# Optimization experiments

Measured on AMD Instinct MI355X. Metric: run time of the kernel, lower is better.

## Reference

```python
import jax, jax.numpy as jnp
import numpy as np

N_NODES = 100000
N_EDGES = 1600000
N_GRAPHS = 256
NODE_F = 92
EDGE_F = 41
HID = 64


def setup_inputs() -> dict:
    key = jax.random.key(0)
    ks = jax.random.split(key, 16)
    Z = 2 * HID + EDGE_F  # 169, concat dim for CGConv
    inp = {
        "x": jax.random.normal(ks[0], (N_NODES, NODE_F), dtype=jnp.float32),
        "edge_index": jax.random.randint(ks[1], (2, N_EDGES), 0, N_NODES, dtype=jnp.int64),
        "edge_attr": jax.random.uniform(ks[2], (N_EDGES, EDGE_F), dtype=jnp.float32),
        "batch": jnp.sort(jax.random.randint(ks[3], (N_NODES,), 0, N_GRAPHS, dtype=jnp.int64)),
        # embedding Linear(node_feat_dim -> hidden)
        "emb_W": jax.random.normal(ks[4], (NODE_F, HID), dtype=jnp.float32) / np.sqrt(NODE_F),
        "emb_b": jnp.zeros((HID,), dtype=jnp.float32),
        # CGConv layer 1: gate (sigmoid) and source (softplus) linears on z=[x_i,x_j,e]
        "c1_Wf": jax.random.normal(ks[5], (Z, HID), dtype=jnp.float32) / np.sqrt(Z),
        "c1_bf": jnp.zeros((HID,), dtype=jnp.float32),
        "c1_Ws": jax.random.normal(ks[6], (Z, HID), dtype=jnp.float32) / np.sqrt(Z),
        "c1_bs": jnp.zeros((HID,), dtype=jnp.float32),
        # CGConv layer 2
        "c2_Wf": jax.random.normal(ks[7], (Z, HID), dtype=jnp.float32) / np.sqrt(Z),
        "c2_bf": jnp.zeros((HID,), dtype=jnp.float32),
        "c2_Ws": jax.random.normal(ks[8], (Z, HID), dtype=jnp.float32) / np.sqrt(Z),
        "c2_bs": jnp.zeros((HID,), dtype=jnp.float32),
        # head
        "l1_W": jax.random.normal(ks[9], (HID, 32), dtype=jnp.float32) / np.sqrt(HID),
        "l1_b": jnp.zeros((32,), dtype=jnp.float32),
        "l2_W": jax.random.normal(ks[10], (32, 2), dtype=jnp.float32) / np.sqrt(32),
        "l2_b": jnp.zeros((2,), dtype=jnp.float32),
    }
    return inp


def _cgconv(x, src, dst, edge_attr, Wf, bf, Ws, bs):
    # PyG CGConv: z = [x_i (target), x_j (source), e_ij]; msg = sigmoid(lin_f(z)) * softplus(lin_s(z))
    z = jnp.concatenate([x[dst], x[src], edge_attr], axis=-1)  # [E, 2H+D]
    msg = jax.nn.sigmoid(z @ Wf + bf) * jax.nn.softplus(z @ Ws + bs)  # [E, H]
    agg = jax.ops.segment_sum(msg, dst, num_segments=x.shape[0])  # scatter-add at targets
    return x + agg  # residual


def reference(x, edge_index, edge_attr, batch,
              emb_W, emb_b, c1_Wf, c1_bf, c1_Ws, c1_bs,
              c2_Wf, c2_bf, c2_Ws, c2_bs, l1_W, l1_b, l2_W, l2_b):
    src = edge_index[0]  # x_j
    dst = edge_index[1]  # x_i
    h = jax.nn.relu(x @ emb_W + emb_b)
    h = jax.nn.relu(_cgconv(h, src, dst, edge_attr, c1_Wf, c1_bf, c1_Ws, c1_bs))
    h = jax.nn.relu(_cgconv(h, src, dst, edge_attr, c2_Wf, c2_bf, c2_Ws, c2_bs))
    # global_mean_pool over graph ids
    sums = jax.ops.segment_sum(h, batch, num_segments=N_GRAPHS)
    cnt = jax.ops.segment_sum(jnp.ones((h.shape[0],), h.dtype), batch, num_segments=N_GRAPHS)
    pooled = sums / jnp.maximum(cnt, 1.0)[:, None]
    g = jax.nn.relu(pooled @ l1_W + l1_b)
    return g @ l2_W + l2_b  # [N_GRAPHS, 2]
```

## Files before the change

kernel.cpp:

```cpp
#include <hip/hip_runtime.h>

#define N_NODES 100000
#define N_EDGES 1600000
#define N_GRAPHS 256
#define NODE_F 92
#define EDGE_F 41
#define HID 64
#define NCHUNK 98

typedef float f2 __attribute__((ext_vector_type(2)));
typedef float f4 __attribute__((ext_vector_type(4)));

__global__ __launch_bounds__(256) void k_embed(const float* __restrict__ x,
                                               const float* __restrict__ W,
                                               const float* __restrict__ b,
                                               float* __restrict__ h) {
    __shared__ float sT[23 * 256];
    for (int i = threadIdx.x; i < 23 * 256; i += 256) {
        const int kq = i >> 8, rem = i & 255, ln = rem >> 2, kk = rem & 3;
        sT[i] = W[(4 * kq + kk) * HID + ln];
    }
    __syncthreads();
    const int lane = threadIdx.x & 63;
    const int nW   = gridDim.x * 4;
    const float bias = b[lane];
    for (int n0 = blockIdx.x * 4 + (threadIdx.x >> 6); n0 < N_NODES; n0 += nW) {
        const int n = __builtin_amdgcn_readfirstlane(n0);
        const float* xr = x + (size_t)n * NODE_F;
        float acc = bias;
#pragma unroll
        for (int k0 = 0; k0 < NODE_F; k0 += 4) {
            const f4 xv = *(const f4*)&xr[k0];
            const f4 wv = *(const f4*)&sT[(k0 >> 2) * 256 + 4 * lane];
            acc = fmaf(xv.x, wv.x, acc);
            acc = fmaf(xv.y, wv.y, acc);
            acc = fmaf(xv.z, wv.z, acc);
            acc = fmaf(xv.w, wv.w, acc);
        }
        h[(size_t)n * HID + lane] = fmaxf(acc, 0.f);
    }
}

__global__ __launch_bounds__(256) void k_hist(const int* __restrict__ ei,
                                              int* __restrict__ cnt) {
    for (int i = blockIdx.x * 256 + threadIdx.x; i < N_EDGES; i += gridDim.x * 256)
        atomicAdd(&cnt[ei[N_EDGES + i]], 1);
}

__global__ __launch_bounds__(256) void k_scan1(const int* __restrict__ cnt,
                                               int* __restrict__ csum) {
    __shared__ int red[256];
    const int b = blockIdx.x, t = threadIdx.x;
    int s = 0;
    for (int i = t; i < 1024; i += 256) {
        const int g = b * 1024 + i;
        s += (g < N_NODES) ? cnt[g] : 0;
    }
    red[t] = s;
    __syncthreads();
    for (int off = 128; off > 0; off >>= 1) {
        if (t < off) red[t] += red[t + off];
        __syncthreads();
    }
    if (t == 0) csum[b] = red[0];
}

__global__ __launch_bounds__(128) void k_scan2(const int* __restrict__ csum,
                                               int* __restrict__ cbase) {
    __shared__ int sh[128];
    const int t = threadIdx.x;
    const int v0 = (t < NCHUNK) ? csum[t] : 0;
    sh[t] = v0;
    __syncthreads();
    for (int off = 1; off < 128; off <<= 1) {
        const int v = (t >= off) ? sh[t - off] : 0;
        __syncthreads();
        sh[t] += v;
        __syncthreads();
    }
    if (t < NCHUNK) cbase[t] = sh[t] - v0;
}

__global__ __launch_bounds__(256) void k_scan3(const int* __restrict__ cnt,
                                               const int* __restrict__ cbase,
                                               int* __restrict__ offs,
                                               int* __restrict__ woffs) {
    __shared__ int sh[256];
    const int b = blockIdx.x, t = threadIdx.x;
    const int g0 = b * 1024 + t * 4;
    int v[4], s = 0;
#pragma unroll
    for (int k = 0; k < 4; ++k) {
        const int g = g0 + k;
        v[k] = (g < N_NODES) ? cnt[g] : 0;
        s += v[k];
    }
    sh[t] = s;
    __syncthreads();
    for (int off = 1; off < 256; off <<= 1) {
        const int x = (t >= off) ? sh[t - off] : 0;
        __syncthreads();
        sh[t] += x;
        __syncthreads();
    }
    int base = cbase[b] + sh[t] - s;
#pragma unroll
    for (int k = 0; k < 4; ++k) {
        const int g = g0 + k;
        if (g < N_NODES) { offs[g] = base; woffs[g] = base; }
        base += v[k];
    }
    if (b == 0 && t == 0) offs[N_NODES] = N_EDGES;
}

__global__ __launch_bounds__(256) void k_scatter(const int* __restrict__ ei,
                                                 int* __restrict__ woffs,
                                                 int2* __restrict__ csr) {
    for (int i = blockIdx.x * 256 + threadIdx.x; i < N_EDGES; i += gridDim.x * 256) {
        const int src = ei[i];
        const int dst = ei[N_EDGES + i];
        const int pos = atomicAdd(&woffs[dst], 1);
        csr[pos] = make_int2(src, i);
    }
}

template <int RELU_IN>
__global__ __launch_bounds__(256) void k_node_pre(const float* hin,
                                                  float* hout,
                                                  const float* __restrict__ Wf,
                                                  const float* __restrict__ Ws,
                                                  float* __restrict__ D,
                                                  float* __restrict__ S) {
    __shared__ float sW[64 * 256];
    for (int i = threadIdx.x; i < 64 * 256; i += 256) {
        const int k = i >> 8, j = i & 255, c = j >> 2, r = j & 3;
        float v;
        if (r == 0)      v = Wf[k * HID + c];
        else if (r == 1) v = Ws[k * HID + c];
        else if (r == 2) v = Wf[(64 + k) * HID + c];
        else             v = Ws[(64 + k) * HID + c];
        sW[i] = v;
    }
    __syncthreads();
    const int lane = threadIdx.x & 63;
    const int wave = blockIdx.x * 4 + (threadIdx.x >> 6);
    const int nW   = gridDim.x * 4;
    for (int base0 = wave * 8; base0 < N_NODES; base0 += nW * 8) {
        const int base = __builtin_amdgcn_readfirstlane(base0);
        float aD0[8] = {}, aD1[8] = {}, aS0[8] = {}, aS1[8] = {};
        for (int k0 = 0; k0 < HID; k0 += 4) {
            f4 wv[4];
#pragma unroll
            for (int kk = 0; kk < 4; ++kk)
                wv[kk] = *(const f4*)&sW[(k0 + kk) * 256 + 4 * lane];
#pragma unroll
            for (int m = 0; m < 8; ++m) {
                f4 hv = *(const f4*)&hin[(size_t)(base + m) * HID + k0];
                if (RELU_IN) {
                    hv.x = fmaxf(hv.x, 0.f); hv.y = fmaxf(hv.y, 0.f);
                    hv.z = fmaxf(hv.z, 0.f); hv.w = fmaxf(hv.w, 0.f);
                }
#pragma unroll
                for (int kk = 0; kk < 4; ++kk) {
                    aD0[m] = fmaf(hv[kk], wv[kk].x, aD0[m]);
                    aD1[m] = fmaf(hv[kk], wv[kk].y, aD1[m]);
                    aS0[m] = fmaf(hv[kk], wv[kk].z, aS0[m]);
                    aS1[m] = fmaf(hv[kk], wv[kk].w, aS1[m]);
                }
            }
        }
#pragma unroll
        for (int m = 0; m < 8; ++m) {
            const size_t n = base + m;
            *(f2*)&D[n * 128 + 2 * lane] = (f2){aD0[m], aD1[m]};
            *(f2*)&S[n * 128 + 2 * lane] = (f2){aS0[m], aS1[m]};
            if (RELU_IN) hout[n * HID + lane] = fmaxf(hin[n * HID + lane], 0.f);
        }
    }
}

__device__ __forceinline__ float act(float f, float s) {
    const float gate = __builtin_amdgcn_rcpf(1.f + __expf(-f));
    const float sp   = fmaxf(s, 0.f) + __logf(1.f + __expf(-fabsf(s)));
    return gate * sp;
}

__global__ __launch_bounds__(256, 4) void k_gather(const int2* __restrict__ csr,
                                                   const int* __restrict__ offs,
                                                   const float* __restrict__ ea,
                                                   const float* __restrict__ D,
                                                   const float* __restrict__ S,
                                                   const float* __restrict__ Wf,
                                                   const float* __restrict__ Ws,
                                                   const float* __restrict__ bf,
                                                   const float* __restrict__ bs,
                                                   const float* hres,
                                                   float* agg) {
    const int lane = threadIdx.x & 63;
    float wf[EDGE_F], ws[EDGE_F];
#pragma unroll
    for (int k = 0; k < EDGE_F; ++k) {
        wf[k] = Wf[(128 + k) * HID + lane];
        ws[k] = Ws[(128 + k) * HID + lane];
    }
    const float bfv = bf[lane], bsv = bs[lane];
    const int nW = gridDim.x * 4;
    for (int n0 = blockIdx.x * 4 + (threadIdx.x >> 6); n0 < N_NODES; n0 += nW) {
        const int n  = __builtin_amdgcn_readfirstlane(n0);
        const int j0 = offs[n];
        const int j1 = offs[n + 1];
        float acc = hres[(size_t)n * HID + lane];
        const f2 dv = *(const f2*)&D[(size_t)n * 128 + 2 * lane];
        const float bD0 = bfv + dv.x, bD1 = bsv + dv.y;
        int j = j0;
        for (; j + 1 < j1; j += 2) {
            const int2 c0 = csr[j], c1 = csr[j + 1];
            const int s0 = __builtin_amdgcn_readfirstlane(c0.x);
            const int e0 = __builtin_amdgcn_readfirstlane(c0.y);
            const int s1 = __builtin_amdgcn_readfirstlane(c1.x);
            const int e1 = __builtin_amdgcn_readfirstlane(c1.y);
            const f2 sv0 = *(const f2*)&S[(size_t)s0 * 128 + 2 * lane];
            const f2 sv1 = *(const f2*)&S[(size_t)s1 * 128 + 2 * lane];
            const float* r0 = ea + (size_t)e0 * EDGE_F;
            const float* r1 = ea + (size_t)e1 * EDGE_F;
            float f0 = bD0 + sv0.x, q0 = bD1 + sv0.y;
            float f1 = bD0 + sv1.x, q1 = bD1 + sv1.y;
#pragma unroll
            for (int k = 0; k < EDGE_F; ++k) {
                const float a = r0[k], b = r1[k];
                f0 = fmaf(a, wf[k], f0); q0 = fmaf(a, ws[k], q0);
                f1 = fmaf(b, wf[k], f1); q1 = fmaf(b, ws[k], q1);
            }
            acc += act(f0, q0) + act(f1, q1);
        }
        if (j < j1) {
            const int2 c0 = csr[j];
            const int s0 = __builtin_amdgcn_readfirstlane(c0.x);
            const int e0 = __builtin_amdgcn_readfirstlane(c0.y);
            const f2 sv0 = *(const f2*)&S[(size_t)s0 * 128 + 2 * lane];
            const float* r0 = ea + (size_t)e0 * EDGE_F;
            float f0 = bD0 + sv0.x, q0 = bD1 + sv0.y;
#pragma unroll
            for (int k = 0; k < EDGE_F; ++k) {
                const float a = r0[k];
                f0 = fmaf(a, wf[k], f0); q0 = fmaf(a, ws[k], q0);
            }
            acc += act(f0, q0);
        }
        agg[(size_t)n * HID + lane] = acc;
    }
}

__global__ __launch_bounds__(256) void k_pool(const float* __restrict__ agg,
                                              const int* __restrict__ batch,
                                              float* __restrict__ psum,
                                              float* __restrict__ pcnt) {
    const int lane = threadIdx.x & 63;
    const int wave = blockIdx.x * 4 + (threadIdx.x >> 6);
    const int nW   = gridDim.x * 4;
    const int chunk = (N_NODES + nW - 1) / nW;
    const int n0 = wave * chunk;
    if (n0 >= N_NODES) return;
    const int n1 = min(n0 + chunk, N_NODES);
    float acc = 0.f;
    int cur = batch[n0];
    int run = 0;
    for (int n = n0; n < n1; ++n) {
        const int g = batch[n];
        if (g != cur) {
            unsafeAtomicAdd(&psum[(size_t)cur * HID + lane], acc);
            if (lane == 0) unsafeAtomicAdd(&pcnt[cur], (float)run);
            acc = 0.f; run = 0; cur = g;
        }
        acc += fmaxf(agg[(size_t)n * HID + lane], 0.f);
        ++run;
    }
    unsafeAtomicAdd(&psum[(size_t)cur * HID + lane], acc);
    if (lane == 0) unsafeAtomicAdd(&pcnt[cur], (float)run);
}

__global__ __launch_bounds__(256) void k_head(const float* __restrict__ psum,
                                              const float* __restrict__ pcnt,
                                              const float* __restrict__ l1W,
                                              const float* __restrict__ l1b,
                                              const float* __restrict__ l2W,
                                              const float* __restrict__ l2b,
                                              float* __restrict__ out) {
    const int g = threadIdx.x;
    const float inv = 1.f / fmaxf(pcnt[g], 1.f);
    float hid[32];
#pragma unroll
    for (int j = 0; j < 32; ++j) hid[j] = l1b[j];
    for (int c = 0; c < HID; ++c) {
        const float pv = psum[(size_t)g * HID + c] * inv;
#pragma unroll
        for (int j = 0; j < 32; ++j) hid[j] = fmaf(pv, l1W[c * 32 + j], hid[j]);
    }
#pragma unroll
    for (int j = 0; j < 32; ++j) hid[j] = fmaxf(hid[j], 0.f);
#pragma unroll
    for (int k = 0; k < 2; ++k) {
        float a = l2b[k];
#pragma unroll
        for (int j = 0; j < 32; ++j) a = fmaf(hid[j], l2W[j * 2 + k], a);
        out[g * 2 + k] = a;
    }
}

extern "C" void kernel_launch(void* const* d_in, const int* in_sizes, int n_in,
                              void* d_out, int out_size, void* d_ws, size_t ws_size,
                              hipStream_t stream) {
    const float* x     = (const float*)d_in[0];
    const int*   ei    = (const int*)d_in[1];
    const float* ea    = (const float*)d_in[2];
    const int*   batch = (const int*)d_in[3];
    const float* embW  = (const float*)d_in[4];
    const float* embb  = (const float*)d_in[5];
    const float* c1Wf  = (const float*)d_in[6];
    const float* c1bf  = (const float*)d_in[7];
    const float* c1Ws  = (const float*)d_in[8];
    const float* c1bs  = (const float*)d_in[9];
    const float* c2Wf  = (const float*)d_in[10];
    const float* c2bf  = (const float*)d_in[11];
    const float* c2Ws  = (const float*)d_in[12];
    const float* c2bs  = (const float*)d_in[13];
    const float* l1W   = (const float*)d_in[14];
    const float* l1b   = (const float*)d_in[15];
    const float* l2W   = (const float*)d_in[16];
    const float* l2b   = (const float*)d_in[17];
    float* out = (float*)d_out;

    char* w = (char*)d_ws;
    float* A    = (float*)w; w += (size_t)N_NODES * HID * sizeof(float);
    float* D    = (float*)w; w += (size_t)N_NODES * 128 * sizeof(float);
    float* S    = (float*)w; w += (size_t)N_NODES * 128 * sizeof(float);
    int2*  csr  = (int2*)w;  w += (size_t)N_EDGES * sizeof(int2);
    int*   cnt  = (int*)w;   w += (size_t)((N_NODES + 4) & ~3) * sizeof(int);
    int*   offs = (int*)w;   w += (size_t)((N_NODES + 4) & ~3) * sizeof(int);
    int*   woffs= (int*)w;   w += (size_t)((N_NODES + 4) & ~3) * sizeof(int);
    int*   csum = (int*)w;   w += 128 * sizeof(int);
    int*   cbase= (int*)w;   w += 128 * sizeof(int);
    float* psum = (float*)w; w += (size_t)N_GRAPHS * HID * sizeof(float);
    float* pcnt = (float*)w; w += (size_t)N_GRAPHS * sizeof(float);

    hipMemsetAsync(cnt, 0, (size_t)N_NODES * sizeof(int), stream);
    hipMemsetAsync(psum, 0, (size_t)(N_GRAPHS * HID + N_GRAPHS) * sizeof(float), stream);

    k_embed<<<1024, 256, 0, stream>>>(x, embW, embb, A);
    k_hist<<<1024, 256, 0, stream>>>(ei, cnt);
    k_scan1<<<NCHUNK, 256, 0, stream>>>(cnt, csum);
    k_scan2<<<1, 128, 0, stream>>>(csum, cbase);
    k_scan3<<<NCHUNK, 256, 0, stream>>>(cnt, cbase, offs, woffs);
    k_scatter<<<1024, 256, 0, stream>>>(ei, woffs, csr);

    k_node_pre<0><<<1024, 256, 0, stream>>>(A, A, c1Wf, c1Ws, D, S);
    k_gather<<<2048, 256, 0, stream>>>(csr, offs, ea, D, S, c1Wf, c1Ws, c1bf, c1bs, A, A);

    k_node_pre<1><<<1024, 256, 0, stream>>>(A, A, c2Wf, c2Ws, D, S);
    k_gather<<<2048, 256, 0, stream>>>(csr, offs, ea, D, S, c2Wf, c2Ws, c2bf, c2bs, A, A);

    k_pool<<<512, 256, 0, stream>>>(A, batch, psum, pcnt);
    k_head<<<1, 256, 0, stream>>>(psum, pcnt, l1W, l1b, l2W, l2b, out);
}
```

Measured before the change: 1.944 ms.

## Use packed FMA in edge gather and merge scan into one kernel

The edge gather now keeps the gate and source weights as packed float2 pairs and uses packed FMA with two interleaved accumulator chains per edge, which halves the FMA instruction count and shortens dependency chains. Launch bounds drop from 4 to 3 waves per SIMD so the packed weights have registers to live in. The three-kernel prefix scan is replaced by a single 1024-thread block scan, removing two launches at the cost of each thread serially walking 98 counts and doing strided, uncoalesced loads.

```diff
diff --git a/kernel.cpp b/kernel.cpp
--- a/kernel.cpp
+++ b/kernel.cpp
@@ -6,10 +6,13 @@
 #define NODE_F 92
 #define EDGE_F 41
 #define HID 64
-#define NCHUNK 98
 
 typedef float f2 __attribute__((ext_vector_type(2)));
 typedef float f4 __attribute__((ext_vector_type(4)));
+
+static __device__ __forceinline__ f2 pk_fma(f2 a, f2 b, f2 c) {
+    return __builtin_elementwise_fma(a, b, c);
+}
 
 __global__ __launch_bounds__(256) void k_embed(const float* __restrict__ x,
                                                const float* __restrict__ W,
@@ -47,70 +50,29 @@
         atomicAdd(&cnt[ei[N_EDGES + i]], 1);
 }
 
-__global__ __launch_bounds__(256) void k_scan1(const int* __restrict__ cnt,
-                                               int* __restrict__ csum) {
-    __shared__ int red[256];
-    const int b = blockIdx.x, t = threadIdx.x;
+__global__ __launch_bounds__(1024) void k_scan(const int* __restrict__ cnt,
+                                               int* __restrict__ offs,
+                                               int* __restrict__ woffs) {
+    __shared__ int sh[1024];
+    const int t  = threadIdx.x;
+    const int c0 = t * 98;
+    const int c1 = min(c0 + 98, N_NODES);
     int s = 0;
-    for (int i = t; i < 1024; i += 256) {
-        const int g = b * 1024 + i;
-        s += (g < N_NODES) ? cnt[g] : 0;
-    }
-    red[t] = s;
+    for (int i = c0; i < c1; ++i) s += cnt[i];
+    sh[t] = s;
     __syncthreads();
-    for (int off = 128; off > 0; off >>= 1) {
-        if (t < off) red[t] += red[t + off];
-        __syncthreads();
-    }
-    if (t == 0) csum[b] = red[0];
-}
-
-__global__ __launch_bounds__(128) void k_scan2(const int* __restrict__ csum,
-                                               int* __restrict__ cbase) {
-    __shared__ int sh[128];
-    const int t = threadIdx.x;
-    const int v0 = (t < NCHUNK) ? csum[t] : 0;
-    sh[t] = v0;
-    __syncthreads();
-    for (int off = 1; off < 128; off <<= 1) {
+    for (int off = 1; off < 1024; off <<= 1) {
         const int v = (t >= off) ? sh[t - off] : 0;
         __syncthreads();
         sh[t] += v;
         __syncthreads();
     }
-    if (t < NCHUNK) cbase[t] = sh[t] - v0;
-}
-
-__global__ __launch_bounds__(256) void k_scan3(const int* __restrict__ cnt,
-                                               const int* __restrict__ cbase,
-                                               int* __restrict__ offs,
-                                               int* __restrict__ woffs) {
-    __shared__ int sh[256];
-    const int b = blockIdx.x, t = threadIdx.x;
-    const int g0 = b * 1024 + t * 4;
-    int v[4], s = 0;
-#pragma unroll
-    for (int k = 0; k < 4; ++k) {
-        const int g = g0 + k;
-        v[k] = (g < N_NODES) ? cnt[g] : 0;
-        s += v[k];
-    }
-    sh[t] = s;
-    __syncthreads();
-    for (int off = 1; off < 256; off <<= 1) {
-        const int x = (t >= off) ? sh[t - off] : 0;
-        __syncthreads();
-        sh[t] += x;
-        __syncthreads();
-    }
-    int base = cbase[b] + sh[t] - s;
-#pragma unroll
-    for (int k = 0; k < 4; ++k) {
-        const int g = g0 + k;
-        if (g < N_NODES) { offs[g] = base; woffs[g] = base; }
-        base += v[k];
-    }
-    if (b == 0 && t == 0) offs[N_NODES] = N_EDGES;
+    int base = sh[t] - s;
+    for (int i = c0; i < c1; ++i) {
+        offs[i] = base; woffs[i] = base;
+        base += cnt[i];
+    }
+    if (t == 0) offs[N_NODES] = N_EDGES;
 }
 
 __global__ __launch_bounds__(256) void k_scatter(const int* __restrict__ ei,
@@ -185,7 +147,7 @@
     return gate * sp;
 }
 
-__global__ __launch_bounds__(256, 4) void k_gather(const int2* __restrict__ csr,
+__global__ __launch_bounds__(256, 3) void k_gather(const int2* __restrict__ csr,
                                                    const int* __restrict__ offs,
                                                    const float* __restrict__ ea,
                                                    const float* __restrict__ D,
@@ -197,13 +159,14 @@
                                                    const float* hres,
                                                    float* agg) {
     const int lane = threadIdx.x & 63;
-    float wf[EDGE_F], ws[EDGE_F];
-#pragma unroll
-    for (int k = 0; k < EDGE_F; ++k) {
-        wf[k] = Wf[(128 + k) * HID + lane];
-        ws[k] = Ws[(128 + k) * HID + lane];
-    }
-    const float bfv = bf[lane], bsv = bs[lane];
+    f2 w2[EDGE_F];
+#pragma unroll
+    for (int k = 0; k < EDGE_F; ++k)
+        w2[k] = (f2){Wf[(128 + k) * HID + lane], Ws[(128 + k) * HID + lane]};
+#pragma unroll
+    for (int k = 0; k < EDGE_F; ++k)
+        asm volatile("" : "+v"(w2[k]));
+    const f2 bias2 = {bf[lane], bs[lane]};
     const int nW = gridDim.x * 4;
     for (int n0 = blockIdx.x * 4 + (threadIdx.x >> 6); n0 < N_NODES; n0 += nW) {
         const int n  = __builtin_amdgcn_readfirstlane(n0);
@@ -211,7 +174,7 @@
         const int j1 = offs[n + 1];
         float acc = hres[(size_t)n * HID + lane];
         const f2 dv = *(const f2*)&D[(size_t)n * 128 + 2 * lane];
-        const float bD0 = bfv + dv.x, bD1 = bsv + dv.y;
+        const f2 nb = bias2 + dv;
         int j = j0;
         for (; j + 1 < j1; j += 2) {
             const int2 c0 = csr[j], c1 = csr[j + 1];
@@ -219,33 +182,47 @@
             const int e0 = __builtin_amdgcn_readfirstlane(c0.y);
             const int s1 = __builtin_amdgcn_readfirstlane(c1.x);
             const int e1 = __builtin_amdgcn_readfirstlane(c1.y);
-            const f2 sv0 = *(const f2*)&S[(size_t)s0 * 128 + 2 * lane];
-            const f2 sv1 = *(const f2*)&S[(size_t)s1 * 128 + 2 * lane];
             const float* r0 = ea + (size_t)e0 * EDGE_F;
             const float* r1 = ea + (size_t)e1 * EDGE_F;
-            float f0 = bD0 + sv0.x, q0 = bD1 + sv0.y;
-            float f1 = bD0 + sv1.x, q1 = bD1 + sv1.y;
-#pragma unroll
-            for (int k = 0; k < EDGE_F; ++k) {
-                const float a = r0[k], b = r1[k];
-                f0 = fmaf(a, wf[k], f0); q0 = fmaf(a, ws[k], q0);
-                f1 = fmaf(b, wf[k], f1); q1 = fmaf(b, ws[k], q1);
+            f2 a0 = nb + *(const f2*)&S[(size_t)s0 * 128 + 2 * lane];
+            f2 a1 = {0.f, 0.f};
+            f2 b0 = nb + *(const f2*)&S[(size_t)s1 * 128 + 2 * lane];
+            f2 b1 = {0.f, 0.f};
+#pragma unroll
+            for (int k = 0; k + 1 < EDGE_F; k += 2) {
+                const float ae = r0[k], ao = r0[k + 1];
+                const float be = r1[k], bo = r1[k + 1];
+                a0 = pk_fma((f2){ae, ae}, w2[k], a0);
+                b0 = pk_fma((f2){be, be}, w2[k], b0);
+                a1 = pk_fma((f2){ao, ao}, w2[k + 1], a1);
+                b1 = pk_fma((f2){bo, bo}, w2[k + 1], b1);
             }
-            acc += act(f0, q0) + act(f1, q1);
+            {
+                const float ae = r0[EDGE_F - 1], be = r1[EDGE_F - 1];
+                a0 = pk_fma((f2){ae, ae}, w2[EDGE_F - 1], a0);
+                b0 = pk_fma((f2){be, be}, w2[EDGE_F - 1], b0);
+            }
+            const f2 fsA = a0 + a1;
+            const f2 fsB = b0 + b1;
+            acc += act(fsA.x, fsA.y) + act(fsB.x, fsB.y);
         }
         if (j < j1) {
             const int2 c0 = csr[j];
             const int s0 = __builtin_amdgcn_readfirstlane(c0.x);
             const int e0 = __builtin_amdgcn_readfirstlane(c0.y);
-            const f2 sv0 = *(const f2*)&S[(size_t)s0 * 128 + 2 * lane];
             const float* r0 = ea + (size_t)e0 * EDGE_F;
-            float f0 = bD0 + sv0.x, q0 = bD1 + sv0.y;
-#pragma unroll
-            for (int k = 0; k < EDGE_F; ++k) {
-                const float a = r0[k];
-                f0 = fmaf(a, wf[k], f0); q0 = fmaf(a, ws[k], q0);
+            f2 a0 = nb + *(const f2*)&S[(size_t)s0 * 128 + 2 * lane];
+            f2 a1 = {0.f, 0.f};
+#pragma unroll
+            for (int k = 0; k + 1 < EDGE_F; k += 2) {
+                const float ae = r0[k], ao = r0[k + 1];
+                a0 = pk_fma((f2){ae, ae}, w2[k], a0);
+                a1 = pk_fma((f2){ao, ao}, w2[k + 1], a1);
             }
-            acc += act(f0, q0);
+            const float ae = r0[EDGE_F - 1];
+            a0 = pk_fma((f2){ae, ae}, w2[EDGE_F - 1], a0);
+            const f2 fs = a0 + a1;
+            acc += act(fs.x, fs.y);
         }
         agg[(size_t)n * HID + lane] = acc;
     }
@@ -338,8 +315,6 @@
     int*   cnt  = (int*)w;   w += (size_t)((N_NODES + 4) & ~3) * sizeof(int);
     int*   offs = (int*)w;   w += (size_t)((N_NODES + 4) & ~3) * sizeof(int);
     int*   woffs= (int*)w;   w += (size_t)((N_NODES + 4) & ~3) * sizeof(int);
-    int*   csum = (int*)w;   w += 128 * sizeof(int);
-    int*   cbase= (int*)w;   w += 128 * sizeof(int);
     float* psum = (float*)w; w += (size_t)N_GRAPHS * HID * sizeof(float);
     float* pcnt = (float*)w; w += (size_t)N_GRAPHS * sizeof(float);
 
@@ -348,9 +323,7 @@
 
     k_embed<<<1024, 256, 0, stream>>>(x, embW, embb, A);
     k_hist<<<1024, 256, 0, stream>>>(ei, cnt);
-    k_scan1<<<NCHUNK, 256, 0, stream>>>(cnt, csum);
-    k_scan2<<<1, 128, 0, stream>>>(csum, cbase);
-    k_scan3<<<NCHUNK, 256, 0, stream>>>(cnt, cbase, offs, woffs);
+    k_scan<<<1, 1024, 0, stream>>>(cnt, offs, woffs);
     k_scatter<<<1024, 256, 0, stream>>>(ei, woffs, csr);
 
     k_node_pre<0><<<1024, 256, 0, stream>>>(A, A, c1Wf, c1Ws, D, S);
```

Measured after the change: 2.005 ms. 3.1% more time.
